# Performance work log

Hardware: AMD Instinct MI355X
Metric: run time of the kernel (lower is better)

## Reference

```python
import jax, jax.numpy as jnp
import numpy as np

N = 50000      # nodes
E = 800000     # edges (last N are self-loops)
F_IN = 128     # n_feats
D = 64         # embedding_size (per-head out dim)
H = 3          # num_heads
G = 1024       # graphs in batch


def setup_inputs() -> dict:
    key = jax.random.key(0)
    ks = jax.random.split(key, 16)
    feats = jax.random.normal(ks[0], (N, F_IN), dtype=jnp.float32)
    # edges: random part + self-loops so every node has in-degree >= 1
    rs = jax.random.randint(ks[1], (E - N,), 0, N)
    rd = jax.random.randint(ks[2], (E - N,), 0, N)
    loops = jnp.arange(N)
    src = jnp.concatenate([rs, loops]).astype(jnp.int32)
    dst = jnp.concatenate([rd, loops]).astype(jnp.int32)
    graph_ids = jnp.sort(jax.random.randint(ks[3], (N,), 0, G)).astype(jnp.int32)

    def nrm(k, shape, fan_in):
        return jax.random.normal(k, shape, dtype=jnp.float32) * (1.0 / np.sqrt(fan_in))

    # gat1A params (DGL GATConv: fc no-bias, attn_l/attn_r [H,D], bias [H*D])
    W1 = nrm(ks[4], (F_IN, H * D), F_IN)
    al1 = nrm(ks[5], (H, D), D)
    ar1 = nrm(ks[6], (H, D), D)
    b1 = jnp.zeros((H * D,), jnp.float32)
    # gatn params (shared across the 2 loop iterations)
    W2 = nrm(ks[7], (D, H * D), D)
    al2 = nrm(ks[8], (H, D), D)
    ar2 = nrm(ks[9], (H, D), D)
    b2 = jnp.zeros((H * D,), jnp.float32)
    # linear1A (shared)
    Wl = nrm(ks[10], (H * D, D), H * D)
    bl = jnp.zeros((D,), jnp.float32)
    return {"feats": feats, "src": src, "dst": dst, "graph_ids": graph_ids,
            "W1": W1, "al1": al1, "ar1": ar1, "b1": b1,
            "W2": W2, "al2": al2, "ar2": ar2, "b2": b2,
            "Wl": Wl, "bl": bl}


def gat_conv(h, W, al, ar, b, src, dst):
    # h: [N, Fin] -> z: [N, H, D]
    z = (h @ W).reshape(-1, H, D)
    el = jnp.sum(z * al, axis=-1)   # [N, H]
    er = jnp.sum(z * ar, axis=-1)   # [N, H]
    e = jax.nn.leaky_relu(el[src] + er[dst], negative_slope=0.2)  # [E, H]
    # edge softmax over incoming edges of each dst node
    m = jax.ops.segment_max(e, dst, num_segments=N)
    ex = jnp.exp(e - m[dst])
    denom = jax.ops.segment_sum(ex, dst, num_segments=N)
    alpha = ex / denom[dst]                              # [E, H]
    msg = z[src] * alpha[:, :, None]                     # [E, H, D]
    out = jax.ops.segment_sum(msg, dst, num_segments=N)  # [N, H, D]
    return out + b.reshape(H, D)


def reference(feats, src, dst, graph_ids, W1, al1, ar1, b1, W2, al2, ar2, b2, Wl, bl):
    x = gat_conv(feats, W1, al1, ar1, b1, src, dst)   # [N, H, D]
    x = x.reshape(N, H * D)
    x = x @ Wl + bl                                   # [N, D]
    for _ in range(2):
        x = gat_conv(x, W2, al2, ar2, b2, src, dst)
        x = x.reshape(N, H * D)
        x = x @ Wl + bl
        # nn.LeakyReLU(True) -> negative_slope = 1.0 -> identity (faithful)
    # AvgPooling: per-graph mean of node features
    sums = jax.ops.segment_sum(x, graph_ids, num_segments=G)           # [G, D]
    cnts = jax.ops.segment_sum(jnp.ones((N,), x.dtype), graph_ids, num_segments=G)
    return sums / jnp.maximum(cnts, 1.0)[:, None]
```

## Files before the change

### kernel.cpp

```cpp
#include <hip/hip_runtime.h>
#include <hip/hip_bf16.h>

#define NN 50000
#define NE 800000
#define FIN 128
#define NHEADS 3
#define NG 1024
#define HD 192

typedef unsigned short ushort_t;
typedef __bf16 bf16x8 __attribute__((ext_vector_type(8)));
typedef float f32x4 __attribute__((ext_vector_type(4)));

__device__ __forceinline__ float bf2f(ushort_t u) {
    union { unsigned int i; float f; } c;
    c.i = ((unsigned int)u) << 16;
    return c.f;
}
__device__ __forceinline__ ushort_t f2bf(float f) {
    __hip_bfloat16 h = __float2bfloat16(f);
    return *reinterpret_cast<ushort_t*>(&h);
}

#define F4 (NN * FIN / 4)
#define W1E (FIN * HD)
#define W2E (64 * HD)
#define WLE (HD * 64)
__global__ __launch_bounds__(256) void conv_all_kernel(const float* __restrict__ feats,
                                                       const float* __restrict__ W1,
                                                       const float* __restrict__ W2,
                                                       const float* __restrict__ Wl,
                                                       ushort_t* __restrict__ featsb,
                                                       ushort_t* __restrict__ W1t,
                                                       ushort_t* __restrict__ W2t,
                                                       ushort_t* __restrict__ Wlt) {
    int i = blockIdx.x * 256 + threadIdx.x;
    if (i < F4) {
        float4 v = ((const float4*)feats)[i];
        ushort4 o;
        o.x = f2bf(v.x); o.y = f2bf(v.y); o.z = f2bf(v.z); o.w = f2bf(v.w);
        ((ushort4*)featsb)[i] = o;
        return;
    }
    int t = i - F4;
    if (t < W1E) {
        int k = t / HD, n = t - k * HD;
        W1t[n * FIN + k] = f2bf(W1[t]);
        return;
    }
    t -= W1E;
    if (t < W2E) {
        int k = t / HD, n = t - k * HD;
        W2t[n * 64 + k] = f2bf(W2[t]);
        return;
    }
    t -= W2E;
    if (t < WLE) {
        int k = t / 64, n = t - k * 64;
        Wlt[n * HD + k] = f2bf(Wl[t]);
    }
}

template<int K, int NT, int ATTN>
__global__ __launch_bounds__(256) void mgemm_kernel(const ushort_t* __restrict__ Ab,
                                                    const ushort_t* __restrict__ Wt,
                                                    const float* __restrict__ bias,
                                                    const float* __restrict__ al,
                                                    const float* __restrict__ ar,
                                                    float* __restrict__ el4,
                                                    float* __restrict__ er4,
                                                    ushort_t* __restrict__ xb,
                                                    ushort_t* __restrict__ zb,
                                                    int nrows) {
    constexpr int N = NT * 16;
    const int lane = threadIdx.x & 63;
    const int wid = threadIdx.x >> 6;
    const int row0 = blockIdx.x * 64 + wid * 16;
    const int m = lane & 15;
    const int kg = lane >> 4;

    int rA = row0 + m;
    if (rA > nrows - 1) rA = nrows - 1;
    const ushort_t* arow = Ab + (size_t)rA * K + kg * 8;

    const f32x4 zero4 = {0.f, 0.f, 0.f, 0.f};
    f32x4 acc[NT];
#pragma unroll
    for (int n = 0; n < NT; ++n) acc[n] = zero4;

#pragma unroll
    for (int k0 = 0; k0 < K; k0 += 32) {
        bf16x8 a = *(const bf16x8*)(arow + k0);
#pragma unroll
        for (int n = 0; n < NT; ++n) {
            bf16x8 b = *(const bf16x8*)(Wt + (size_t)(n * 16 + m) * K + k0 + kg * 8);
            acc[n] = __builtin_amdgcn_mfma_f32_16x16x32_bf16(a, b, acc[n], 0, 0, 0);
        }
    }

    const int orow = row0 + kg * 4;

    if (ATTN) {
        float sl[NHEADS][4], sr[NHEADS][4];
#pragma unroll
        for (int h = 0; h < NHEADS; ++h)
#pragma unroll
            for (int r = 0; r < 4; ++r) { sl[h][r] = 0.f; sr[h][r] = 0.f; }
#pragma unroll
        for (int n = 0; n < NT; ++n) {
            float alv = al[n * 16 + m];
            float arv = ar[n * 16 + m];
            const int h = n >> 2;
#pragma unroll
            for (int r = 0; r < 4; ++r) {
                sl[h][r] = fmaf(acc[n][r], alv, sl[h][r]);
                sr[h][r] = fmaf(acc[n][r], arv, sr[h][r]);
            }
        }
#pragma unroll
        for (int off = 1; off < 16; off <<= 1) {
#pragma unroll
            for (int h = 0; h < NHEADS; ++h)
#pragma unroll
                for (int r = 0; r < 4; ++r) {
                    sl[h][r] += __shfl_xor(sl[h][r], off);
                    sr[h][r] += __shfl_xor(sr[h][r], off);
                }
        }
#pragma unroll
        for (int r = 0; r < 4; ++r) {
            int gr = orow + r;
            if (gr < nrows) {
#pragma unroll
                for (int n = 0; n < NT; ++n)
                    zb[(size_t)gr * N + n * 16 + m] = f2bf(acc[n][r]);
                if (m == 0) {
                    *(float4*)(el4 + (size_t)gr * 4) = make_float4(sl[0][r], sl[1][r], sl[2][r], 0.f);
                    *(float4*)(er4 + (size_t)gr * 4) = make_float4(sr[0][r], sr[1][r], sr[2][r], 0.f);
                }
            }
        }
    } else {
#pragma unroll
        for (int r = 0; r < 4; ++r) {
            int gr = orow + r;
            if (gr < nrows) {
#pragma unroll
                for (int n = 0; n < NT; ++n)
                    xb[(size_t)gr * N + n * 16 + m] = f2bf(acc[n][r] + bias[n * 16 + m]);
            }
        }
    }
}

__global__ __launch_bounds__(256) void count_kernel(const int* __restrict__ dst,
                                                    int* __restrict__ cnt,
                                                    int* __restrict__ rank) {
    int e0 = blockIdx.x * 1024 + threadIdx.x;
#pragma unroll
    for (int k = 0; k < 4; ++k) {
        int e = e0 + k * 256;
        if (e < NE) rank[e] = atomicAdd(&cnt[dst[e]], 1);
    }
}

__global__ __launch_bounds__(256) void scan_block_kernel(const int* __restrict__ cnt,
                                                         int* __restrict__ incl,
                                                         int* __restrict__ bsum, int n) {
    __shared__ int s[256];
    int tid = threadIdx.x;
    int i = blockIdx.x * 256 + tid;
    int v = (i < n) ? cnt[i] : 0;
    s[tid] = v;
    __syncthreads();
#pragma unroll
    for (int off = 1; off < 256; off <<= 1) {
        int add = (tid >= off) ? s[tid - off] : 0;
        __syncthreads();
        s[tid] += add;
        __syncthreads();
    }
    if (i < n) incl[i] = s[tid];
    if (tid == 255) bsum[blockIdx.x] = s[255];
}

__global__ __launch_bounds__(256) void finalize_rowptr_kernel(const int* __restrict__ incl,
                                                              const int* __restrict__ bsum,
                                                              int* __restrict__ row_ptr, int n) {
    int b = blockIdx.x;
    int part = 0;
    for (int k = (threadIdx.x & 63); k < b; k += 64) part += bsum[k];
#pragma unroll
    for (int off = 32; off > 0; off >>= 1) part += __shfl_xor(part, off);
    int i = b * 256 + threadIdx.x;
    if (i < n) row_ptr[i + 1] = incl[i] + part;
    if (i == 0) row_ptr[0] = 0;
}

__global__ __launch_bounds__(256) void fill_kernel(const int* __restrict__ src,
                                                   const int* __restrict__ dst,
                                                   const int* __restrict__ row_ptr,
                                                   const int* __restrict__ rank,
                                                   int* __restrict__ srcs_sorted) {
    int e = blockIdx.x * 256 + threadIdx.x;
    if (e < NE) {
        srcs_sorted[row_ptr[dst[e]] + rank[e]] = src[e];
    }
}

__global__ __launch_bounds__(256) void aggregate_kernel(const ushort_t* __restrict__ zb,
                                                        const float* __restrict__ el4,
                                                        const float* __restrict__ er4,
                                                        const int* __restrict__ row_ptr,
                                                        const int* __restrict__ srcs,
                                                        const float* __restrict__ bias,
                                                        ushort_t* __restrict__ yb) {
    __shared__ float plds[4][NHEADS][72];
    int node = blockIdx.x * 4 + (threadIdx.x >> 6);
    int lane = threadIdx.x & 63;
    if (node >= NN) return;
    int s0 = row_ptr[node], s1 = row_ptr[node + 1];
    size_t o = (size_t)node * HD;
    const int wid = threadIdx.x >> 6;
    const int h = lane >> 4;
    const int loff = lane * 4;

    float4 erv = *(const float4*)(er4 + (size_t)node * 4);

    float d0 = 0.f, d1 = 0.f, d2 = 0.f;
    f32x4 a = {0.f, 0.f, 0.f, 0.f};

    for (int c0 = s0; c0 < s1; c0 += 64) {
        int i = c0 + lane;
        float p0 = 0.f, p1 = 0.f, p2 = 0.f;
        int s = 0;
        if (i < s1) {
            s = srcs[i];
            float4 elv = *(const float4*)(el4 + (size_t)s * 4);
            float e0 = elv.x + erv.x, e1 = elv.y + erv.y, e2 = elv.z + erv.z;
            e0 = e0 > 0.f ? e0 : 0.2f * e0;
            e1 = e1 > 0.f ? e1 : 0.2f * e1;
            e2 = e2 > 0.f ? e2 : 0.2f * e2;
            p0 = __expf(fminf(e0, 60.f));
            p1 = __expf(fminf(e1, 60.f));
            p2 = __expf(fminf(e2, 60.f));
        }
        d0 += p0; d1 += p1; d2 += p2;
        plds[wid][0][lane] = p0;
        plds[wid][1][lane] = p1;
        plds[wid][2][lane] = p2;
        asm volatile("s_waitcnt lgkmcnt(0)" ::: "memory");
        int nch = s1 - c0; if (nch > 64) nch = 64;
        if (lane < 48) {
            const float* prow = &plds[wid][h][0];
            for (int j = 0; j < nch; j += 8) {
                ushort4 zv[8];
#pragma unroll
                for (int t = 0; t < 8; ++t) {
                    int sj = __builtin_amdgcn_readlane(s, j + t);
                    zv[t] = *(const ushort4*)(zb + (size_t)sj * HD + loff);
                }
                float4 qa = *(const float4*)(prow + j);
                float4 qb = *(const float4*)(prow + j + 4);
                float qq[8] = {qa.x, qa.y, qa.z, qa.w, qb.x, qb.y, qb.z, qb.w};
#pragma unroll
                for (int t = 0; t < 8; ++t) {
                    a[0] = fmaf(qq[t], bf2f(zv[t].x), a[0]);
                    a[1] = fmaf(qq[t], bf2f(zv[t].y), a[1]);
                    a[2] = fmaf(qq[t], bf2f(zv[t].z), a[2]);
                    a[3] = fmaf(qq[t], bf2f(zv[t].w), a[3]);
                }
            }
        }
    }
#pragma unroll
    for (int off = 32; off > 0; off >>= 1) {
        d0 += __shfl_xor(d0, off);
        d1 += __shfl_xor(d1, off);
        d2 += __shfl_xor(d2, off);
    }

    if (lane < 48) {
        float dd = (h == 0) ? d0 : ((h == 1) ? d1 : d2);
        float rinv = 1.0f / dd;
        float4 bb = *(const float4*)(bias + loff);
        ushort4 ov;
        ov.x = f2bf(a[0] * rinv + bb.x);
        ov.y = f2bf(a[1] * rinv + bb.y);
        ov.z = f2bf(a[2] * rinv + bb.z);
        ov.w = f2bf(a[3] * rinv + bb.w);
        *(ushort4*)(yb + o + loff) = ov;
    }
}

__global__ __launch_bounds__(256) void pool_kernel(const ushort_t* __restrict__ xb,
                                                   const int* __restrict__ gid,
                                                   float* __restrict__ gsum,
                                                   int* __restrict__ gcnt) {
    int w = blockIdx.x * 4 + (threadIdx.x >> 6);
    int lane = threadIdx.x & 63;
    int n0 = w * 16;
    if (n0 >= NN) return;
    int n1 = n0 + 16; if (n1 > NN) n1 = NN;
    int curg = gid[n0];
    float acc = 0.f;
    int cl = 0;
    for (int n = n0; n < n1; ++n) {
        int g = gid[n];
        if (g != curg) {
            atomicAdd(&gsum[curg * 64 + lane], acc);
            if (lane == 0) atomicAdd(&gcnt[curg], cl);
            acc = 0.f; cl = 0; curg = g;
        }
        acc += bf2f(xb[(size_t)n * 64 + lane]);
        cl++;
    }
    atomicAdd(&gsum[curg * 64 + lane], acc);
    if (lane == 0) atomicAdd(&gcnt[curg], cl);
}

__global__ __launch_bounds__(256) void pool_final_kernel(const float* __restrict__ gsum,
                                                         const int* __restrict__ gcnt,
                                                         float* __restrict__ out) {
    int idx = blockIdx.x * 256 + threadIdx.x;
    if (idx < NG * 64) {
        int g = idx >> 6;
        float c = (float)gcnt[g];
        out[idx] = gsum[idx] / fmaxf(c, 1.0f);
    }
}

extern "C" void kernel_launch(void* const* d_in, const int* in_sizes, int n_in,
                              void* d_out, int out_size, void* d_ws, size_t ws_size,
                              hipStream_t stream) {
    const float* feats = (const float*)d_in[0];
    const int* src = (const int*)d_in[1];
    const int* dst = (const int*)d_in[2];
    const int* gid = (const int*)d_in[3];
    const float* W1 = (const float*)d_in[4];
    const float* al1 = (const float*)d_in[5];
    const float* ar1 = (const float*)d_in[6];
    const float* b1 = (const float*)d_in[7];
    const float* W2 = (const float*)d_in[8];
    const float* al2 = (const float*)d_in[9];
    const float* ar2 = (const float*)d_in[10];
    const float* b2 = (const float*)d_in[11];
    const float* Wl = (const float*)d_in[12];
    const float* bl = (const float*)d_in[13];
    float* out = (float*)d_out;

    size_t off = 0;
    auto alloc = [&](size_t bytes) -> char* {
        char* p = (char*)d_ws + off;
        off += (bytes + 255) & ~(size_t)255;
        return p;
    };
    ushort_t* featsb = (ushort_t*)alloc((size_t)NN * FIN * 2);
    ushort_t* zb = (ushort_t*)alloc((size_t)NN * HD * 2);
    ushort_t* yb = (ushort_t*)alloc((size_t)NN * HD * 2);
    ushort_t* xb = (ushort_t*)alloc((size_t)NN * 64 * 2);
    float* el4 = (float*)alloc((size_t)NN * 4 * 4);
    float* er4 = (float*)alloc((size_t)NN * 4 * 4);
    ushort_t* W1t = (ushort_t*)alloc((size_t)HD * FIN * 2);
    ushort_t* W2t = (ushort_t*)alloc((size_t)HD * 64 * 2);
    ushort_t* Wlt = (ushort_t*)alloc((size_t)64 * HD * 2);
    int* row_ptr = (int*)alloc((size_t)(NN + 1) * 4);
    int* cnt = (int*)alloc((size_t)NN * 4);
    int* incl = (int*)alloc((size_t)NN * 4);
    int* bsum = (int*)alloc(256 * 4);
    int* rank = (int*)alloc((size_t)NE * 4);
    int* srcs = (int*)alloc((size_t)NE * 4);
    float* gsum = (float*)alloc((size_t)NG * 64 * 4);
    int* gcnt = (int*)alloc((size_t)NG * 4);

    const int nbScan = (NN + 255) / 256;
    const int gridE = (NE + 255) / 256;
    const int gridNode = (NN + 3) / 4;
    const int gridGemm = (NN + 63) / 64;

    conv_all_kernel<<<(F4 + W1E + W2E + WLE + 255) / 256, 256, 0, stream>>>(
        feats, W1, W2, Wl, featsb, W1t, W2t, Wlt);

    hipMemsetAsync(cnt, 0, (size_t)NN * 4, stream);
    count_kernel<<<(NE + 1023) / 1024, 256, 0, stream>>>(dst, cnt, rank);
    scan_block_kernel<<<nbScan, 256, 0, stream>>>(cnt, incl, bsum, NN);
    finalize_rowptr_kernel<<<nbScan, 256, 0, stream>>>(incl, bsum, row_ptr, NN);
    fill_kernel<<<gridE, 256, 0, stream>>>(src, dst, row_ptr, rank, srcs);

    mgemm_kernel<FIN, 12, 1><<<gridGemm, 256, 0, stream>>>(featsb, W1t, nullptr, al1, ar1,
                                                           el4, er4, nullptr, zb, NN);
    aggregate_kernel<<<gridNode, 256, 0, stream>>>(zb, el4, er4, row_ptr, srcs, b1, yb);
    mgemm_kernel<HD, 4, 0><<<gridGemm, 256, 0, stream>>>(yb, Wlt, bl, nullptr, nullptr,
                                                         nullptr, nullptr, xb, nullptr, NN);

    for (int it = 0; it < 2; ++it) {
        mgemm_kernel<64, 12, 1><<<gridGemm, 256, 0, stream>>>(xb, W2t, nullptr, al2, ar2,
                                                              el4, er4, nullptr, zb, NN);
        aggregate_kernel<<<gridNode, 256, 0, stream>>>(zb, el4, er4, row_ptr, srcs, b2, yb);
        mgemm_kernel<HD, 4, 0><<<gridGemm, 256, 0, stream>>>(yb, Wlt, bl, nullptr, nullptr,
                                                             nullptr, nullptr, xb, nullptr, NN);
    }

    hipMemsetAsync(gsum, 0, (size_t)NG * 64 * 4 + (size_t)NG * 4, stream);
    pool_kernel<<<(NN / 16 + 3) / 4 + 1, 256, 0, stream>>>(xb, gid, gsum, gcnt);
    pool_final_kernel<<<(NG * 64 + 255) / 256, 256, 0, stream>>>(gsum, gcnt, out);
}
```

Measured before the change: 418.1 us.

## Split aggregate gather into two edge halves with 16-byte loads per lane

The aggregation kernel now lets each of 24 lanes cover 8 bf16 features of a 192-wide row with one 16-byte load, and splits the 48 active lanes into two groups that handle even and odd edges in parallel. The partial sums are combined with a cross-lane shuffle before normalisation and the bias add. This widens each gather load and halves the serial edge loop per lane, at the cost of 8 accumulators, a cross-lane reduction, and odd-count edge handling that depends on zero padding in the probability buffer.

```diff
diff --git a/kernel.cpp b/kernel.cpp
--- a/kernel.cpp
+++ b/kernel.cpp
@@ -15,6 +15,16 @@
 __device__ __forceinline__ float bf2f(ushort_t u) {
     union { unsigned int i; float f; } c;
     c.i = ((unsigned int)u) << 16;
+    return c.f;
+}
+__device__ __forceinline__ float bf2f_lo(unsigned int u) {
+    union { unsigned int i; float f; } c;
+    c.i = u << 16;
+    return c.f;
+}
+__device__ __forceinline__ float bf2f_hi(unsigned int u) {
+    union { unsigned int i; float f; } c;
+    c.i = u & 0xffff0000u;
     return c.f;
 }
 __device__ __forceinline__ ushort_t f2bf(float f) {
@@ -222,13 +232,17 @@
     int s0 = row_ptr[node], s1 = row_ptr[node + 1];
     size_t o = (size_t)node * HD;
     const int wid = threadIdx.x >> 6;
-    const int h = lane >> 4;
-    const int loff = lane * 4;
+    const int g24 = (lane < 48) ? (lane < 24 ? lane : lane - 24) : 0;
+    const int halfE = (lane >= 24) ? 1 : 0;
+    const int h = g24 >> 3;
+    const int uoff = g24 * 8;
 
     float4 erv = *(const float4*)(er4 + (size_t)node * 4);
 
     float d0 = 0.f, d1 = 0.f, d2 = 0.f;
-    f32x4 a = {0.f, 0.f, 0.f, 0.f};
+    float a[8];
+#pragma unroll
+    for (int t = 0; t < 8; ++t) a[t] = 0.f;
 
     for (int c0 = s0; c0 < s1; c0 += 64) {
         int i = c0 + lane;
@@ -252,24 +266,22 @@
         asm volatile("s_waitcnt lgkmcnt(0)" ::: "memory");
         int nch = s1 - c0; if (nch > 64) nch = 64;
         if (lane < 48) {
-            const float* prow = &plds[wid][h][0];
-            for (int j = 0; j < nch; j += 8) {
-                ushort4 zv[8];
-#pragma unroll
-                for (int t = 0; t < 8; ++t) {
-                    int sj = __builtin_amdgcn_readlane(s, j + t);
-                    zv[t] = *(const ushort4*)(zb + (size_t)sj * HD + loff);
-                }
-                float4 qa = *(const float4*)(prow + j);
-                float4 qb = *(const float4*)(prow + j + 4);
-                float qq[8] = {qa.x, qa.y, qa.z, qa.w, qb.x, qb.y, qb.z, qb.w};
-#pragma unroll
-                for (int t = 0; t < 8; ++t) {
-                    a[0] = fmaf(qq[t], bf2f(zv[t].x), a[0]);
-                    a[1] = fmaf(qq[t], bf2f(zv[t].y), a[1]);
-                    a[2] = fmaf(qq[t], bf2f(zv[t].z), a[2]);
-                    a[3] = fmaf(qq[t], bf2f(zv[t].w), a[3]);
-                }
+            const float* prow = &plds[wid][h][halfE];
+#pragma unroll 4
+            for (int j = 0; j < nch; j += 2) {
+                int sjA = __builtin_amdgcn_readlane(s, j);
+                int sjB = __builtin_amdgcn_readlane(s, j + 1);
+                int sj = halfE ? sjB : sjA;
+                uint4 zv = *(const uint4*)(zb + (size_t)sj * HD + uoff);
+                float q = prow[j];
+                a[0] = fmaf(q, bf2f_lo(zv.x), a[0]);
+                a[1] = fmaf(q, bf2f_hi(zv.x), a[1]);
+                a[2] = fmaf(q, bf2f_lo(zv.y), a[2]);
+                a[3] = fmaf(q, bf2f_hi(zv.y), a[3]);
+                a[4] = fmaf(q, bf2f_lo(zv.z), a[4]);
+                a[5] = fmaf(q, bf2f_hi(zv.z), a[5]);
+                a[6] = fmaf(q, bf2f_lo(zv.w), a[6]);
+                a[7] = fmaf(q, bf2f_hi(zv.w), a[7]);
             }
         }
     }
@@ -279,17 +291,25 @@
         d1 += __shfl_xor(d1, off);
         d2 += __shfl_xor(d2, off);
     }
-
-    if (lane < 48) {
+#pragma unroll
+    for (int t = 0; t < 8; ++t) a[t] += __shfl_down(a[t], 24);
+
+    if (lane < 24) {
         float dd = (h == 0) ? d0 : ((h == 1) ? d1 : d2);
         float rinv = 1.0f / dd;
-        float4 bb = *(const float4*)(bias + loff);
-        ushort4 ov;
-        ov.x = f2bf(a[0] * rinv + bb.x);
-        ov.y = f2bf(a[1] * rinv + bb.y);
-        ov.z = f2bf(a[2] * rinv + bb.z);
-        ov.w = f2bf(a[3] * rinv + bb.w);
-        *(ushort4*)(yb + o + loff) = ov;
+        float4 bb0 = *(const float4*)(bias + uoff);
+        float4 bb1 = *(const float4*)(bias + uoff + 4);
+        ushort4 ov0, ov1;
+        ov0.x = f2bf(a[0] * rinv + bb0.x);
+        ov0.y = f2bf(a[1] * rinv + bb0.y);
+        ov0.z = f2bf(a[2] * rinv + bb0.z);
+        ov0.w = f2bf(a[3] * rinv + bb0.w);
+        ov1.x = f2bf(a[4] * rinv + bb1.x);
+        ov1.y = f2bf(a[5] * rinv + bb1.y);
+        ov1.z = f2bf(a[6] * rinv + bb1.z);
+        ov1.w = f2bf(a[7] * rinv + bb1.w);
+        *(ushort4*)(yb + o + uoff) = ov0;
+        *(ushort4*)(yb + o + uoff + 4) = ov1;
     }
 }
 
```

Result: slower. 435.0 us (+4.1%).
